# Kernel tuning notes

Hardware: AMD Instinct MI355X
Metric: run time of the kernel (lower is better)

## Reference

```python
import jax, jax.numpy as jnp
import numpy as np

V = 25  # number of skeleton joints (hard-coded in the original module)

def setup_inputs() -> dict:
    key = jax.random.key(0)
    k1, k2 = jax.random.split(key)
    shape = (256, 3, 600, 25, 2)  # N, C, T, V, M
    x = jax.random.normal(k1, shape, dtype=jnp.float32)
    y = jax.random.normal(k2, shape, dtype=jnp.float32)
    return {"x": x, "y": y}

def reference(x, y):
    # x, y: (N, C, T, V, M)
    # temporal motion: difference along T
    motion = x[:, :, 1:, :, :] - x[:, :, :-1, :, :]            # (N, C, T-1, V, M)
    # per-(sample, joint) mean absolute motion over C, T-1, M
    mean_move = jnp.mean(jnp.abs(motion), axis=(1, 2, 4))      # (N, V)
    # normalize per sample so ratios sum to V (=25)
    ratio = V * mean_move / jnp.sum(mean_move, axis=1, keepdims=True)  # (N, V)
    # weighted squared error, mean over all elements
    sq = (x - y) ** 2                                          # (N, C, T, V, M)
    weighted = sq * ratio[:, None, None, :, None]
    return jnp.mean(weighted)
```

## Files before the change

### kernel.cpp

```cpp
#include <hip/hip_runtime.h>

#define N_ 256
#define C_ 3
#define T_ 600
#define V_ 25
#define TG 60
#define TILES_PER_SLAB 5
#define NBLK (N_ * C_ * TILES_PER_SLAB)

__global__ __launch_bounds__(256, 4) void slab_kernel(const float* __restrict__ x,
                                                      const float* __restrict__ y,
                                                      float* __restrict__ absws,
                                                      float* __restrict__ sqws) {
    __shared__ float xt[TG * 100];
    __shared__ float bnd[50];
    __shared__ float binAbs[32], binSq[32];

    const int t    = threadIdx.x;
    const int bid  = blockIdx.x;
    const int slab = bid / TILES_PER_SLAB;
    const int tile = bid % TILES_PER_SLAB;
    const int G0   = tile * TG;
    const int n    = slab / C_;

    if (t < 32) { binAbs[t] = 0.f; binSq[t] = 0.f; }

    const bool active = (t < 250);
    const int p = t % 25;
    const int g = t / 25;

    const float4* __restrict__ xs4 = reinterpret_cast<const float4*>(x) + (size_t)slab * 7500 + (size_t)G0 * 25;
    const float4* __restrict__ ys4 = reinterpret_cast<const float4*>(y) + (size_t)slab * 7500 + (size_t)G0 * 25;

    float sqA = 0.f, sqB = 0.f;

    if (active) {
        #pragma unroll
        for (int h = 0; h < 2; ++h) {
            float4 xv[3], yv[3];
            #pragma unroll
            for (int k = 0; k < 3; ++k) {
                const int rp = (h * 3 + k) * 10 + g;
                xv[k] = xs4[rp * 25 + p];
                yv[k] = ys4[rp * 25 + p];
            }
            #pragma unroll
            for (int k = 0; k < 3; ++k) {
                const int rp = (h * 3 + k) * 10 + g;
                *reinterpret_cast<float4*>(&xt[rp * 100 + 4 * p]) = xv[k];
                const float e0 = xv[k].x - yv[k].x, e1 = xv[k].y - yv[k].y;
                const float e2 = xv[k].z - yv[k].z, e3 = xv[k].w - yv[k].w;
                sqA += e0 * e0 + e1 * e1;
                sqB += e2 * e2 + e3 * e3;
            }
        }
    }
    if (G0 > 0 && t < 25) {
        const float2* b2 = reinterpret_cast<const float2*>(x) + (size_t)slab * 15000 + (size_t)(2 * G0 - 1) * 25;
        reinterpret_cast<float2*>(bnd)[t] = b2[t];
    }
    __syncthreads();

    if (active) {
        const int v = p;
        const int c = g;
        int j0 = 12 * c;
        const int j1 = j0 + 12;
        const float2* rows = reinterpret_cast<const float2*>(xt);
        float2 prev;
        if (j0 == 0) {
            if (G0 > 0) prev = reinterpret_cast<const float2*>(bnd)[v];
            else { prev = rows[v]; j0 = 1; }
        } else {
            prev = rows[(j0 - 1) * 25 + v];
        }
        float mot = 0.f;
        #pragma unroll
        for (int j = j0; j < j1; ++j) {
            const float2 cur = rows[j * 25 + v];
            mot += fabsf(cur.x - prev.x) + fabsf(cur.y - prev.y);
            prev = cur;
        }
        atomicAdd(&binAbs[v], mot);
        const int vA = (p < 12) ? 2 * p     : (p == 12 ? 24 : 2 * p - 25);
        const int vB = (p < 12) ? 2 * p + 1 : (p == 12 ? 0  : 2 * p - 24);
        atomicAdd(&binSq[vA], sqA);
        atomicAdd(&binSq[vB], sqB);
    }
    __syncthreads();

    if (t < V_) {
        atomicAdd(&absws[n * V_ + t], binAbs[t]);
        atomicAdd(&sqws[n * V_ + t], binSq[t]);
    }
}

__global__ __launch_bounds__(256) void finalize_kernel(const float* __restrict__ absws,
                                                       const float* __restrict__ sqws,
                                                       float* __restrict__ out) {
    const int n = threadIdx.x;
    float sumAbs = 0.0f;
    #pragma unroll
    for (int v = 0; v < V_; ++v) sumAbs += absws[n * V_ + v];
    float sumW = 0.0f;
    #pragma unroll
    for (int v = 0; v < V_; ++v) sumW += absws[n * V_ + v] * sqws[n * V_ + v];
    float partial = (float)V_ * sumW / sumAbs;

    __shared__ float red[256];
    red[n] = partial;
    __syncthreads();
    for (int s = 128; s > 0; s >>= 1) {
        if (n < s) red[n] += red[n + s];
        __syncthreads();
    }
    if (n == 0) out[0] = red[0] / (float)((size_t)N_ * C_ * T_ * 25 * 2);
}

extern "C" void kernel_launch(void* const* d_in, const int* in_sizes, int n_in,
                              void* d_out, int out_size, void* d_ws, size_t ws_size,
                              hipStream_t stream) {
    const float* x = (const float*)d_in[0];
    const float* y = (const float*)d_in[1];
    float* out   = (float*)d_out;
    float* absws = (float*)d_ws;
    float* sqws  = absws + N_ * V_;

    hipMemsetAsync(d_ws, 0, (size_t)(2 * N_ * V_) * sizeof(float), stream);

    slab_kernel<<<NBLK, 256, 0, stream>>>(x, y, absws, sqws);

    finalize_kernel<<<1, 256, 0, stream>>>(absws, sqws, out);
}
```

Measured before the change: 42.96 us.

## Compute temporal motion in registers without shared-memory staging tile

After: 50.27 us. +17.0%, slower.

```diff
diff --git a/kernel.cpp b/kernel.cpp
--- a/kernel.cpp
+++ b/kernel.cpp
@@ -4,88 +4,93 @@
 #define C_ 3
 #define T_ 600
 #define V_ 25
-#define TG 60
-#define TILES_PER_SLAB 5
-#define NBLK (N_ * C_ * TILES_PER_SLAB)
+#define GPP 15
+#define UPS (300 / GPP)
+#define UPB 10
+#define NBLK (N_ * C_ * UPS / UPB)
 
-__global__ __launch_bounds__(256, 4) void slab_kernel(const float* __restrict__ x,
-                                                      const float* __restrict__ y,
-                                                      float* __restrict__ absws,
-                                                      float* __restrict__ sqws) {
-    __shared__ float xt[TG * 100];
-    __shared__ float bnd[50];
+__global__ __launch_bounds__(256) void slab_kernel(const float* __restrict__ x,
+                                                   const float* __restrict__ y,
+                                                   float* __restrict__ absws,
+                                                   float* __restrict__ sqws) {
     __shared__ float binAbs[32], binSq[32];
+    const int t = threadIdx.x;
+    if (t < 32) { binAbs[t] = 0.f; binSq[t] = 0.f; }
+    __syncthreads();
 
-    const int t    = threadIdx.x;
-    const int bid  = blockIdx.x;
-    const int slab = bid / TILES_PER_SLAB;
-    const int tile = bid % TILES_PER_SLAB;
-    const int G0   = tile * TG;
-    const int n    = slab / C_;
+    const int  unitg  = blockIdx.x * UPB + t / V_;
+    const int  p      = t % V_;
+    const bool active = (t < UPB * V_);
+    const int  slab   = unitg / UPS;
+    const int  n      = slab / C_;
+    const int  g0     = (unitg % UPS) * GPP;
 
-    if (t < 32) { binAbs[t] = 0.f; binSq[t] = 0.f; }
-
-    const bool active = (t < 250);
-    const int p = t % 25;
-    const int g = t / 25;
-
-    const float4* __restrict__ xs4 = reinterpret_cast<const float4*>(x) + (size_t)slab * 7500 + (size_t)G0 * 25;
-    const float4* __restrict__ ys4 = reinterpret_cast<const float4*>(y) + (size_t)slab * 7500 + (size_t)G0 * 25;
-
-    float sqA = 0.f, sqB = 0.f;
+    float sqA = 0.f, sqB = 0.f, mA = 0.f, mB = 0.f;
 
     if (active) {
-        #pragma unroll
-        for (int h = 0; h < 2; ++h) {
-            float4 xv[3], yv[3];
+        const float* __restrict__ xs = x + (size_t)slab * 30000;
+        const float* __restrict__ ys = y + (size_t)slab * 30000;
+        const int e4 = 4 * p;
+
+        float c0 = 0.f, c1 = 0.f, c2 = 0.f, c3 = 0.f;
+        bool first = true;
+
+        for (int b = 0; b < GPP; b += 5) {
+            float4 xf[5], yf[5];
+            float2 fa[5], fb[5];
             #pragma unroll
-            for (int k = 0; k < 3; ++k) {
-                const int rp = (h * 3 + k) * 10 + g;
-                xv[k] = xs4[rp * 25 + p];
-                yv[k] = ys4[rp * 25 + p];
+            for (int k = 0; k < 5; ++k) {
+                const int g = g0 + b + k;
+                const float* pb = xs + g * 100;
+                xf[k] = *reinterpret_cast<const float4*>(pb + e4);
+                yf[k] = *reinterpret_cast<const float4*>(ys + g * 100 + e4);
+                if (p <= 11) {
+                    fa[k] = *reinterpret_cast<const float2*>(pb + 50 + e4);
+                    fb[k] = *reinterpret_cast<const float2*>(pb + 52 + e4);
+                } else if (p == 12) {
+                    fa[k] = *reinterpret_cast<const float2*>(pb + 98);
+                }
             }
             #pragma unroll
-            for (int k = 0; k < 3; ++k) {
-                const int rp = (h * 3 + k) * 10 + g;
-                *reinterpret_cast<float4*>(&xt[rp * 100 + 4 * p]) = xv[k];
-                const float e0 = xv[k].x - yv[k].x, e1 = xv[k].y - yv[k].y;
-                const float e2 = xv[k].z - yv[k].z, e3 = xv[k].w - yv[k].w;
+            for (int k = 0; k < 5; ++k) {
+                const float4 a = xf[k], q = yf[k];
+                const float e0 = a.x - q.x, e1 = a.y - q.y;
+                const float e2 = a.z - q.z, e3 = a.w - q.w;
                 sqA += e0 * e0 + e1 * e1;
                 sqB += e2 * e2 + e3 * e3;
+                if (p <= 11) {
+                    mA += fabsf(fa[k].x - a.x) + fabsf(fa[k].y - a.y);
+                    mB += fabsf(fb[k].x - a.z) + fabsf(fb[k].y - a.w);
+                    if (!first) {
+                        mA += fabsf(a.x - c0) + fabsf(a.y - c1);
+                        mB += fabsf(a.z - c2) + fabsf(a.w - c3);
+                    }
+                    c0 = fa[k].x; c1 = fa[k].y; c2 = fb[k].x; c3 = fb[k].y;
+                } else if (p == 12) {
+                    mA += fabsf(fa[k].x - a.x) + fabsf(fa[k].y - a.y);
+                    if (!first) {
+                        mA += fabsf(a.x - c0) + fabsf(a.y - c1);
+                    }
+                    c0 = fa[k].x; c1 = fa[k].y;
+                }
+                first = false;
             }
         }
-    }
-    if (G0 > 0 && t < 25) {
-        const float2* b2 = reinterpret_cast<const float2*>(x) + (size_t)slab * 15000 + (size_t)(2 * G0 - 1) * 25;
-        reinterpret_cast<float2*>(bnd)[t] = b2[t];
-    }
-    __syncthreads();
 
-    if (active) {
-        const int v = p;
-        const int c = g;
-        int j0 = 12 * c;
-        const int j1 = j0 + 12;
-        const float2* rows = reinterpret_cast<const float2*>(xt);
-        float2 prev;
-        if (j0 == 0) {
-            if (G0 > 0) prev = reinterpret_cast<const float2*>(bnd)[v];
-            else { prev = rows[v]; j0 = 1; }
-        } else {
-            prev = rows[(j0 - 1) * 25 + v];
+        if (g0 + GPP < 300 && p <= 12) {
+            const float4 s = *reinterpret_cast<const float4*>(xs + (size_t)(g0 + GPP) * 100 + e4);
+            mA += fabsf(s.x - c0) + fabsf(s.y - c1);
+            if (p <= 11) mB += fabsf(s.z - c2) + fabsf(s.w - c3);
         }
-        float mot = 0.f;
-        #pragma unroll
-        for (int j = j0; j < j1; ++j) {
-            const float2 cur = rows[j * 25 + v];
-            mot += fabsf(cur.x - prev.x) + fabsf(cur.y - prev.y);
-            prev = cur;
+
+        const int jA = (p <= 11) ? 2 * p     : (p == 12 ? 24 : 2 * p - 25);
+        const int jB = (p <= 11) ? 2 * p + 1 : (p == 12 ? 0  : 2 * p - 24);
+        atomicAdd(&binSq[jA], sqA);
+        atomicAdd(&binSq[jB], sqB);
+        if (p <= 12) {
+            atomicAdd(&binAbs[jA], mA);
+            if (p <= 11) atomicAdd(&binAbs[jB], mB);
         }
-        atomicAdd(&binAbs[v], mot);
-        const int vA = (p < 12) ? 2 * p     : (p == 12 ? 24 : 2 * p - 25);
-        const int vB = (p < 12) ? 2 * p + 1 : (p == 12 ? 0  : 2 * p - 24);
-        atomicAdd(&binSq[vA], sqA);
-        atomicAdd(&binSq[vB], sqB);
     }
     __syncthreads();
 
@@ -114,7 +119,7 @@
         if (n < s) red[n] += red[n + s];
         __syncthreads();
     }
-    if (n == 0) out[0] = red[0] / (float)((size_t)N_ * C_ * T_ * 25 * 2);
+    if (n == 0) out[0] = red[0] / (float)((size_t)N_ * C_ * T_ * V_ * 2);
 }
 
 extern "C" void kernel_launch(void* const* d_in, const int* in_sizes, int n_in,
```
